# Optimization experiments

Hardware: AMD Instinct MI355X
Metric: run time of the kernel (lower is better)

Reference implementation:

```python
import jax, jax.numpy as jnp
import numpy as np

EPS = 1e-5

def _bn(x, g, b):
    # BatchNorm3d in training mode over (batch, spatial) dims; x: [B, C, N]
    mean = jnp.mean(x, axis=(0, 2), keepdims=True)
    var = jnp.var(x, axis=(0, 2), keepdims=True)
    return g[None, :, None] * (x - mean) * jax.lax.rsqrt(var + EPS) + b[None, :, None]


def setup_inputs() -> dict:
    key = jax.random.key(0)
    ks = jax.random.split(key, 6)
    B, C, N, K, H = 2, 128, 32768, 9, 512
    x = jax.random.normal(ks[0], (B, C, N, 1), dtype=jnp.float32)
    edge_index = jax.random.randint(ks[1], (2, B, N, K), 0, N, dtype=jnp.int32)
    s = 0.05
    return {
        "x": x,
        "edge_index": edge_index,
        "w_mr": jax.random.normal(ks[2], (C, 2 * C), dtype=jnp.float32) * s,
        "b_mr": jnp.zeros((C,), jnp.float32),
        "g_mr": jnp.ones((C,), jnp.float32),
        "be_mr": jnp.zeros((C,), jnp.float32),
        "w1": jax.random.normal(ks[3], (H, C), dtype=jnp.float32) * s,
        "b1": jnp.zeros((H,), jnp.float32),
        "g1": jnp.ones((H,), jnp.float32),
        "be1": jnp.zeros((H,), jnp.float32),
        "w2": jax.random.normal(ks[4], (C, H), dtype=jnp.float32) * s,
        "b2": jnp.zeros((C,), jnp.float32),
        "g2": jnp.ones((C,), jnp.float32),
        "be2": jnp.zeros((C,), jnp.float32),
    }


def reference(x, edge_index, w_mr, b_mr, g_mr, be_mr, w1, b1, g1, be1, w2, b2, g2, be2):
    # x: [B, C, N, 1], edge_index: [2, B, N, K]
    B, C, N, _ = x.shape
    x2 = x[..., 0]  # [B, C, N]

    # batched_index_select: gather node features along N for each (B, N, K) index
    gather = jax.vmap(lambda xb, ib: xb[:, ib])  # ([C,N],[N,K]) -> [C,N,K]
    x_i = gather(x2, edge_index[1])  # [B, C, N, K] center features
    x_j = gather(x2, edge_index[0])  # [B, C, N, K] neighbor features
    rel = jnp.max(x_j - x_i, axis=-1)  # max-relative reduction -> [B, C, N]

    # torch.cat([x.unsqueeze(2), rel.unsqueeze(2)], 2).reshape(B, 2C, N): interleaved channels
    feat = jnp.stack([x2, rel], axis=2).reshape(B, 2 * C, N)

    # BasicConv([2C, C]): Conv3d 1x1 -> BN -> ReLU
    y = jnp.einsum('oc,bcn->bon', w_mr, feat) + b_mr[None, :, None]
    y = jax.nn.relu(_bn(y, g_mr, be_mr))

    # FFN: conv1x1 C->H, BN, ReLU, conv1x1 H->C, BN, residual
    h = jnp.einsum('hc,bcn->bhn', w1, y) + b1[None, :, None]
    h = jax.nn.relu(_bn(h, g1, be1))
    out = jnp.einsum('ch,bhn->bcn', w2, h) + b2[None, :, None]
    out = _bn(out, g2, be2) + y
    return out  # [B, C, N]
```

## Files before the change

### kernel.cpp

```cpp
#include <hip/hip_runtime.h>
#include <hip/hip_bf16.h>
#include <cstddef>
#include <cstdint>

#define BB 2
#define CC 128
#define NN 32768
#define KNBR 9
#define HH 512
#define PP (BB * NN)
#define TWO_C 256
#define EPSBN 1e-5f

typedef __attribute__((ext_vector_type(4))) float f32x4;
typedef __attribute__((ext_vector_type(8))) short s16x8;

__device__ __forceinline__ float bf2f(unsigned int u) {
    return __uint_as_float(u << 16);
}
__device__ __forceinline__ unsigned short f2bf(float f) {
    unsigned int u = __float_as_uint(f);
    u += 0x7fffu + ((u >> 16) & 1u);
    return (unsigned short)(u >> 16);
}

__device__ __forceinline__ s16x8 bnrelu(s16x8 v, f32x4 sa0, f32x4 sa1,
                                        f32x4 sb0, f32x4 sb1) {
    union { s16x8 s; __hip_bfloat162 h[4]; } u;
    u.s = v;
#pragma unroll
    for (int q = 0; q < 4; q++) {
        const float2 f = __bfloat1622float2(u.h[q]);
        const float slo = (q < 2) ? sa0[2 * q] : sa1[2 * q - 4];
        const float shi = (q < 2) ? sa0[2 * q + 1] : sa1[2 * q - 3];
        const float tlo = (q < 2) ? sb0[2 * q] : sb1[2 * q - 4];
        const float thi = (q < 2) ? sb0[2 * q + 1] : sb1[2 * q - 3];
        u.h[q] = __float22bfloat162_rn(make_float2(
            fmaxf(fmaf(slo, f.x, tlo), 0.f), fmaxf(fmaf(shi, f.y, thi), 0.f)));
    }
    return u.s;
}


__global__ __launch_bounds__(256) void transpose_kernel(
    const float* __restrict__ x, unsigned short* __restrict__ xT) {
    __shared__ float t[32][129];
    const int b = blockIdx.y;
    const int n0 = blockIdx.x * 32;
    const int tid = threadIdx.x;
    {
        const int tn = tid % 32;
        const int cq = tid / 32;
        for (int c = cq; c < CC; c += 8)
            t[tn][c] = x[((size_t)b * CC + c) * NN + n0 + tn];
    }
    __syncthreads();
    {
        const int ct = tid % 128;
        const int nq = tid / 128;
        for (int nl = nq; nl < 32; nl += 2)
            xT[((size_t)b * NN + n0 + nl) * CC + ct] = f2bf(t[nl][ct]);
    }
}

__global__ __launch_bounds__(256) void gather_kernel(
    const unsigned short* __restrict__ xT, const int* __restrict__ ei,
    unsigned short* __restrict__ feat) {
    __shared__ unsigned short lds[16 * 264];
    const int p0 = blockIdx.x * 16;
    const int b = p0 >> 15;
    const int n0 = p0 & (NN - 1);
    const int tid = threadIdx.x;
    const int wv = tid >> 6, lane = tid & 63;
    const unsigned short* xb = xT + (size_t)b * NN * CC;

#pragma unroll
    for (int q = 0; q < 4; q++) {
        const int pl = wv * 4 + q;
        const int n = n0 + pl;
        const int* e0 = ei + ((size_t)b * NN + n) * KNBR;
        const int* e1 = ei + ((size_t)(BB + b) * NN + n) * KNBR;
        const unsigned int xv = *(const unsigned int*)(xb + (size_t)n * CC + lane * 2);
        float m0 = -INFINITY, m1 = -INFINITY;
#pragma unroll
        for (int k = 0; k < KNBR; k++) {
            const int j0 = e0[k], j1 = e1[k];
            const unsigned int va = *(const unsigned int*)(xb + (size_t)j0 * CC + lane * 2);
            const unsigned int vb = *(const unsigned int*)(xb + (size_t)j1 * CC + lane * 2);
            m0 = fmaxf(m0, bf2f(va & 0xffffu) - bf2f(vb & 0xffffu));
            m1 = fmaxf(m1, bf2f(va >> 16) - bf2f(vb >> 16));
        }
        ushort4 o;
        o.x = (unsigned short)(xv & 0xffffu);
        o.y = f2bf(m0);
        o.z = (unsigned short)(xv >> 16);
        o.w = f2bf(m1);
        *(ushort4*)(lds + pl * 264 + lane * 4) = o;
    }
    __syncthreads();
#pragma unroll
    for (int pass = 0; pass < 2; pass++) {
        const int s = pass * 256 + tid;
        const int kt = s >> 6, ln = s & 63;
        const int pl = ln & 15, kq = ln >> 4;
        const s16x8 v = *(const s16x8*)(lds + pl * 264 + kt * 32 + kq * 8);
        *(s16x8*)(feat + ((size_t)((p0 >> 4) * 8 + kt) * 64 + ln) * 8) = v;
    }
}

__global__ __launch_bounds__(256) void wconv_kernel(
    const float* __restrict__ w_mr, const float* __restrict__ w1,
    const float* __restrict__ w2, unsigned short* __restrict__ o_mr,
    unsigned short* __restrict__ o1, unsigned short* __restrict__ o2) {
    const int t = blockIdx.x * 256 + threadIdx.x;
    const float* src; unsigned short* dst; int K; int slot;
    if (t < 8192) { src = w1; dst = o1; K = 128; slot = t; }
    else if (t < 16384) { src = w2; dst = o2; K = 512; slot = t - 8192; }
    else if (t < 20480) { src = w_mr; dst = o_mr; K = 256; slot = t - 16384; }
    else return;
    const int lane = slot & 63;
    const int kt = (slot >> 6) % (K / 32);
    const int ot = (slot >> 6) / (K / 32);
    const int oc = ot * 16 + (lane & 15);
    const int k0 = kt * 32 + (lane >> 4) * 8;
    s16x8 v;
#pragma unroll
    for (int j = 0; j < 8; j++) v[j] = (short)f2bf(src[(size_t)oc * K + k0 + j]);
    *(s16x8*)(dst + (size_t)slot * 8) = v;
}

template <int KTOT, int OCB, int OC, bool ACT>
__global__ __launch_bounds__(256, 2) void sgemm2_kernel(
    const unsigned short* __restrict__ A,
    const unsigned short* __restrict__ W,
    const float* __restrict__ bias,
    const float* __restrict__ act,
    unsigned short* __restrict__ Cout,
    float* __restrict__ part) {
    constexpr int KT = KTOT / 32;
    constexpr int NTB = OCB / 16;
    constexpr int NTW = NTB / 2;
    constexpr int OCT32 = OC / 32;

    __shared__ __align__(16) unsigned short ALDS[4 * KT * 512];
    __shared__ float bs[4 * OCB];

    const int tid = threadIdx.x;
    const int w = tid >> 6, lane = tid & 63;
    const int mw = w >> 1, nw = w & 1;
    const int lm = lane & 15, lg = lane >> 4;
    const int pt0 = blockIdx.x * 4;
    const int ob = blockIdx.y * OCB;

    {
        const unsigned short* Asrc = A + (size_t)pt0 * KT * 512;
        s16x8 ar[KT];
#pragma unroll
        for (int i = 0; i < KT; i++)
            ar[i] = *(const s16x8*)(Asrc + (size_t)(i * 256 + tid) * 8);
#pragma unroll
        for (int i = 0; i < KT; i++)
            *(s16x8*)(ALDS + (size_t)(i * 256 + tid) * 8) = ar[i];
    }
    __syncthreads();

    f32x4 acc[2][NTW] = {};

#pragma unroll
    for (int kt = 0; kt < KT; kt++) {
        s16x8 bF[NTW];
#pragma unroll
        for (int n = 0; n < NTW; n++)
            bF[n] = *(const s16x8*)(
                W + ((size_t)(((ob >> 4) + nw * NTW + n) * KT + kt) * 64 + lane) * 8);
        s16x8 a0 = *(const s16x8*)(ALDS + (size_t)(((mw * 2 + 0) * KT + kt) * 64 + lane) * 8);
        s16x8 a1 = *(const s16x8*)(ALDS + (size_t)(((mw * 2 + 1) * KT + kt) * 64 + lane) * 8);
        if (ACT) {
            const int ke = kt * 32 + lg * 8;
            const f32x4 xa0 = *(const f32x4*)(act + ke);
            const f32x4 xa1 = *(const f32x4*)(act + ke + 4);
            const f32x4 xb0 = *(const f32x4*)(act + KTOT + ke);
            const f32x4 xb1 = *(const f32x4*)(act + KTOT + ke + 4);
            a0 = bnrelu(a0, xa0, xa1, xb0, xb1);
            a1 = bnrelu(a1, xa0, xa1, xb0, xb1);
        }
#pragma unroll
        for (int n = 0; n < NTW; n++) {
            acc[0][n] = __builtin_amdgcn_mfma_f32_16x16x32_bf16(a0, bF[n], acc[0][n], 0, 0, 0);
            acc[1][n] = __builtin_amdgcn_mfma_f32_16x16x32_bf16(a1, bF[n], acc[1][n], 0, 0, 0);
        }
    }
    __syncthreads();

    unsigned short* myct = ALDS + (size_t)w * (NTW / 2) * 512;
    float sA[NTW], sB[NTW], bo[NTW];
#pragma unroll
    for (int n = 0; n < NTW; n++) {
        sA[n] = 0.f; sB[n] = 0.f;
        bo[n] = bias[ob + nw * (OCB / 2) + n * 16 + lm];
    }
#pragma unroll
    for (int mi = 0; mi < 2; mi++) {
        const int ptile = pt0 + mw * 2 + mi;
#pragma unroll
        for (int n = 0; n < NTW; n++) {
            const int lbase = ((n & 1) * 2 + (lm >> 3)) * 16 + lg * 4;
            const int elem = lm & 7;
#pragma unroll
            for (int j = 0; j < 4; j++) {
                const float h = acc[mi][n][j] + bo[n];
                sA[n] += h;
                sB[n] = fmaf(h, h, sB[n]);
                myct[(size_t)((n >> 1) * 64 + lbase + j) * 8 + elem] = f2bf(h);
            }
        }
#pragma unroll
        for (int og = 0; og < NTW / 2; og++) {
            const s16x8 v = *(const s16x8*)(myct + (size_t)(og * 64 + lane) * 8);
            const int oct = ((ob + nw * (OCB / 2)) >> 5) + og;
            *(s16x8*)(Cout + ((size_t)(ptile * OCT32 + oct) * 64 + lane) * 8) = v;
        }
    }
#pragma unroll
    for (int n = 0; n < NTW; n++) {
        float a = sA[n], q = sB[n];
        a += __shfl_xor(a, 16); a += __shfl_xor(a, 32);
        q += __shfl_xor(q, 16); q += __shfl_xor(q, 32);
        if (lg == 0) {
            const int chl = nw * (OCB / 2) + n * 16 + lm;
            bs[(mw * 2 + 0) * OCB + chl] = a;
            bs[(mw * 2 + 1) * OCB + chl] = q;
        }
    }
    __syncthreads();
    if (tid < OCB) {
        const float s = bs[0 * OCB + tid] + bs[2 * OCB + tid];
        const float q = bs[1 * OCB + tid] + bs[3 * OCB + tid];
        const size_t o = ((size_t)blockIdx.y * gridDim.x + blockIdx.x) * 2 * OCB;
        part[o + tid] = s;
        part[o + OCB + tid] = q;
    }
}

template <int OCB, int GX>
__global__ __launch_bounds__(256) void reduce_kernel(
    const float* __restrict__ part, const float* __restrict__ g,
    const float* __restrict__ be, float* __restrict__ act, int OC, float invP) {
    __shared__ float ls[4], lq[4];
    const int c = blockIdx.x;
    const int by = c / OCB, co = c % OCB;
    const int tid = threadIdx.x;
    float s = 0.f, q = 0.f;
#pragma unroll
    for (int i = 0; i < GX / 256; i++) {
        const int bx = i * 256 + tid;
        const size_t o = (size_t)(by * GX + bx) * 2 * OCB;
        s += part[o + co];
        q += part[o + OCB + co];
    }
#pragma unroll
    for (int off = 32; off >= 1; off >>= 1) {
        s += __shfl_xor(s, off);
        q += __shfl_xor(q, off);
    }
    if ((tid & 63) == 0) { ls[tid >> 6] = s; lq[tid >> 6] = q; }
    __syncthreads();
    if (tid == 0) {
        s = ls[0] + ls[1] + ls[2] + ls[3];
        q = lq[0] + lq[1] + lq[2] + lq[3];
        const float mean = s * invP;
        const float var = q * invP - mean * mean;
        const float a = g[c] * rsqrtf(var + EPSBN);
        act[c] = a;
        act[OC + c] = be[c] - mean * a;
    }
}

__global__ __launch_bounds__(256) void final_kernel(
    const unsigned short* __restrict__ yF, const unsigned short* __restrict__ oF,
    const float* __restrict__ act1, const float* __restrict__ act3,
    float* __restrict__ out) {
    __shared__ float t[32][132];
    const int p0 = blockIdx.x * 32;
    const int b = p0 >> 15;
    const int n0 = p0 & (NN - 1);
    const int tid = threadIdx.x;
#pragma unroll
    for (int s = tid; s < 512; s += 256) {
        const int pt = s >> 8;
        const int kt = (s >> 6) & 3;
        const int lane = s & 63;
        const int nl = pt * 16 + (lane & 15);
        const int c0 = kt * 32 + (lane >> 4) * 8;
        const size_t off = ((size_t)(((p0 >> 4) + pt) * 4 + kt) * 64 + lane) * 8;
        const s16x8 yv = *(const s16x8*)(yF + off);
        const s16x8 ov = *(const s16x8*)(oF + off);
        const f32x4 a1lo = *(const f32x4*)(act1 + c0);
        const f32x4 a1hi = *(const f32x4*)(act1 + c0 + 4);
        const f32x4 b1lo = *(const f32x4*)(act1 + CC + c0);
        const f32x4 b1hi = *(const f32x4*)(act1 + CC + c0 + 4);
        const f32x4 a3lo = *(const f32x4*)(act3 + c0);
        const f32x4 a3hi = *(const f32x4*)(act3 + c0 + 4);
        const f32x4 b3lo = *(const f32x4*)(act3 + CC + c0);
        const f32x4 b3hi = *(const f32x4*)(act3 + CC + c0 + 4);
#pragma unroll
        for (int j = 0; j < 8; j++) {
            const float yf = bf2f((unsigned short)yv[j]);
            const float of = bf2f((unsigned short)ov[j]);
            const float a1 = (j < 4) ? a1lo[j] : a1hi[j - 4];
            const float b1 = (j < 4) ? b1lo[j] : b1hi[j - 4];
            const float a3 = (j < 4) ? a3lo[j] : a3hi[j - 4];
            const float b3 = (j < 4) ? b3lo[j] : b3hi[j - 4];
            t[nl][c0 + j] = fmaf(a3, of, b3) + fmaxf(fmaf(a1, yf, b1), 0.f);
        }
    }
    __syncthreads();
    const int tn = tid & 31;
    const int cq = tid >> 5;
    for (int c = cq; c < CC; c += 8)
        out[((size_t)b * CC + c) * NN + n0 + tn] = t[tn][c];
}

extern "C" void kernel_launch(void* const* d_in, const int* in_sizes, int n_in,
                              void* d_out, int out_size, void* d_ws, size_t ws_size,
                              hipStream_t stream) {
    const float* x     = (const float*)d_in[0];
    const int*   ei    = (const int*)d_in[1];
    const float* w_mr  = (const float*)d_in[2];
    const float* b_mr  = (const float*)d_in[3];
    const float* g_mr  = (const float*)d_in[4];
    const float* be_mr = (const float*)d_in[5];
    const float* w1    = (const float*)d_in[6];
    const float* b1    = (const float*)d_in[7];
    const float* g1    = (const float*)d_in[8];
    const float* be1   = (const float*)d_in[9];
    const float* w2    = (const float*)d_in[10];
    const float* b2    = (const float*)d_in[11];
    const float* g2    = (const float*)d_in[12];
    const float* be2   = (const float*)d_in[13];
    float* out = (float*)d_out;

    char* ws = (char*)d_ws;
    unsigned short* xT    = (unsigned short*)(ws + 0);
    unsigned short* featF = (unsigned short*)(ws + 16777216);
    unsigned short* yF    = (unsigned short*)(ws + 50331648);
    unsigned short* hF    = (unsigned short*)(ws + 67108864);
    unsigned short* oF    = (unsigned short*)(ws + 134217728);
    unsigned short* wmrF  = (unsigned short*)(ws + 150994944);
    unsigned short* w1F   = (unsigned short*)(ws + 151060480);
    unsigned short* w2F   = (unsigned short*)(ws + 151191552);
    float* act1  = (float*)(ws + 151322624);
    float* act2  = (float*)(ws + 151323648);
    float* act3  = (float*)(ws + 151327744);
    float* part1 = (float*)(ws + 67108864);
    float* part2 = (float*)(ws + 134217728);
    float* part3 = (float*)(ws + 16777216);

    const float invP = 1.0f / (float)PP;

    transpose_kernel<<<dim3(NN / 32, BB), 256, 0, stream>>>(x, xT);
    gather_kernel<<<PP / 16, 256, 0, stream>>>(xT, ei, featF);
    wconv_kernel<<<80, 256, 0, stream>>>(w_mr, w1, w2, wmrF, w1F, w2F);

    sgemm2_kernel<TWO_C, CC, CC, false><<<dim3(PP / 64, 1), 256, 0, stream>>>(
        featF, wmrF, b_mr, act1, yF, part1);
    reduce_kernel<CC, PP / 64><<<CC, 256, 0, stream>>>(
        part1, g_mr, be_mr, act1, CC, invP);

    sgemm2_kernel<CC, 256, HH, true><<<dim3(PP / 64, 2), 256, 0, stream>>>(
        yF, w1F, b1, act1, hF, part2);
    reduce_kernel<256, PP / 64><<<HH, 256, 0, stream>>>(
        part2, g1, be1, act2, HH, invP);

    sgemm2_kernel<HH, CC, CC, true><<<dim3(PP / 64, 1), 256, 0, stream>>>(
        hF, w2F, b2, act2, oF, part3);
    reduce_kernel<CC, PP / 64><<<CC, 256, 0, stream>>>(
        part3, g2, be2, act3, CC, invP);

    final_kernel<<<PP / 32, 256, 0, stream>>>(yF, oF, act1, act3, out);
}
```

Before: 155.2 us.

## Replace BN partial-sum reduce kernels with atomics and move BN-ReLU to A-tile load

Each GEMM block now accumulates its per-channel sum and sum-of-squares directly into a global stats buffer with atomicAdd, and a tiny finalize kernel computes the scale and shift. This replaces the per-block partial write and the separate reduce kernel. The weight conversion is folded into the transpose launch as extra blocks. BN+ReLU on the A operand is applied once when the tile is staged into LDS instead of on every MFMA k-step. Atomics make the float summation order nondeterministic and add contention, and a memset is needed each call.

New measurement: 218.8 us. 1.41x slower.

```diff
diff --git a/kernel.cpp b/kernel.cpp
--- a/kernel.cpp
+++ b/kernel.cpp
@@ -42,8 +42,30 @@
 }
 
 
-__global__ __launch_bounds__(256) void transpose_kernel(
-    const float* __restrict__ x, unsigned short* __restrict__ xT) {
+__global__ __launch_bounds__(256) void transpose_wconv_kernel(
+    const float* __restrict__ x, unsigned short* __restrict__ xT,
+    const float* __restrict__ w_mr, const float* __restrict__ w1,
+    const float* __restrict__ w2, unsigned short* __restrict__ o_mr,
+    unsigned short* __restrict__ o1, unsigned short* __restrict__ o2) {
+    if (blockIdx.x >= NN / 32) {
+        if (blockIdx.y != 0) return;
+        const int t = (blockIdx.x - NN / 32) * 256 + threadIdx.x;
+        const float* src; unsigned short* dst; int K; int slot;
+        if (t < 8192) { src = w1; dst = o1; K = 128; slot = t; }
+        else if (t < 16384) { src = w2; dst = o2; K = 512; slot = t - 8192; }
+        else if (t < 20480) { src = w_mr; dst = o_mr; K = 256; slot = t - 16384; }
+        else return;
+        const int lane = slot & 63;
+        const int kt = (slot >> 6) % (K / 32);
+        const int ot = (slot >> 6) / (K / 32);
+        const int oc = ot * 16 + (lane & 15);
+        const int k0 = kt * 32 + (lane >> 4) * 8;
+        s16x8 v;
+#pragma unroll
+        for (int j = 0; j < 8; j++) v[j] = (short)f2bf(src[(size_t)oc * K + k0 + j]);
+        *(s16x8*)(dst + (size_t)slot * 8) = v;
+        return;
+    }
     __shared__ float t[32][129];
     const int b = blockIdx.y;
     const int n0 = blockIdx.x * 32;
@@ -108,27 +130,6 @@
     }
 }
 
-__global__ __launch_bounds__(256) void wconv_kernel(
-    const float* __restrict__ w_mr, const float* __restrict__ w1,
-    const float* __restrict__ w2, unsigned short* __restrict__ o_mr,
-    unsigned short* __restrict__ o1, unsigned short* __restrict__ o2) {
-    const int t = blockIdx.x * 256 + threadIdx.x;
-    const float* src; unsigned short* dst; int K; int slot;
-    if (t < 8192) { src = w1; dst = o1; K = 128; slot = t; }
-    else if (t < 16384) { src = w2; dst = o2; K = 512; slot = t - 8192; }
-    else if (t < 20480) { src = w_mr; dst = o_mr; K = 256; slot = t - 16384; }
-    else return;
-    const int lane = slot & 63;
-    const int kt = (slot >> 6) % (K / 32);
-    const int ot = (slot >> 6) / (K / 32);
-    const int oc = ot * 16 + (lane & 15);
-    const int k0 = kt * 32 + (lane >> 4) * 8;
-    s16x8 v;
-#pragma unroll
-    for (int j = 0; j < 8; j++) v[j] = (short)f2bf(src[(size_t)oc * K + k0 + j]);
-    *(s16x8*)(dst + (size_t)slot * 8) = v;
-}
-
 template <int KTOT, int OCB, int OC, bool ACT>
 __global__ __launch_bounds__(256, 2) void sgemm2_kernel(
     const unsigned short* __restrict__ A,
@@ -136,7 +137,7 @@
     const float* __restrict__ bias,
     const float* __restrict__ act,
     unsigned short* __restrict__ Cout,
-    float* __restrict__ part) {
+    float* __restrict__ stats) {
     constexpr int KT = KTOT / 32;
     constexpr int NTB = OCB / 16;
     constexpr int NTW = NTB / 2;
@@ -158,6 +159,20 @@
 #pragma unroll
         for (int i = 0; i < KT; i++)
             ar[i] = *(const s16x8*)(Asrc + (size_t)(i * 256 + tid) * 8);
+        if (ACT) {
+#pragma unroll
+            for (int i = 0; i < KT; i++) {
+                const int s = i * 256 + tid;
+                const int kts = (s >> 6) % KT;
+                const int lgs = (s & 63) >> 4;
+                const int ke = kts * 32 + lgs * 8;
+                const f32x4 xa0 = *(const f32x4*)(act + ke);
+                const f32x4 xa1 = *(const f32x4*)(act + ke + 4);
+                const f32x4 xb0 = *(const f32x4*)(act + KTOT + ke);
+                const f32x4 xb1 = *(const f32x4*)(act + KTOT + ke + 4);
+                ar[i] = bnrelu(ar[i], xa0, xa1, xb0, xb1);
+            }
+        }
 #pragma unroll
         for (int i = 0; i < KT; i++)
             *(s16x8*)(ALDS + (size_t)(i * 256 + tid) * 8) = ar[i];
@@ -173,17 +188,8 @@
         for (int n = 0; n < NTW; n++)
             bF[n] = *(const s16x8*)(
                 W + ((size_t)(((ob >> 4) + nw * NTW + n) * KT + kt) * 64 + lane) * 8);
-        s16x8 a0 = *(const s16x8*)(ALDS + (size_t)(((mw * 2 + 0) * KT + kt) * 64 + lane) * 8);
-        s16x8 a1 = *(const s16x8*)(ALDS + (size_t)(((mw * 2 + 1) * KT + kt) * 64 + lane) * 8);
-        if (ACT) {
-            const int ke = kt * 32 + lg * 8;
-            const f32x4 xa0 = *(const f32x4*)(act + ke);
-            const f32x4 xa1 = *(const f32x4*)(act + ke + 4);
-            const f32x4 xb0 = *(const f32x4*)(act + KTOT + ke);
-            const f32x4 xb1 = *(const f32x4*)(act + KTOT + ke + 4);
-            a0 = bnrelu(a0, xa0, xa1, xb0, xb1);
-            a1 = bnrelu(a1, xa0, xa1, xb0, xb1);
-        }
+        const s16x8 a0 = *(const s16x8*)(ALDS + (size_t)(((mw * 2 + 0) * KT + kt) * 64 + lane) * 8);
+        const s16x8 a1 = *(const s16x8*)(ALDS + (size_t)(((mw * 2 + 1) * KT + kt) * 64 + lane) * 8);
 #pragma unroll
         for (int n = 0; n < NTW; n++) {
             acc[0][n] = __builtin_amdgcn_mfma_f32_16x16x32_bf16(a0, bF[n], acc[0][n], 0, 0, 0);
@@ -236,43 +242,22 @@
     if (tid < OCB) {
         const float s = bs[0 * OCB + tid] + bs[2 * OCB + tid];
         const float q = bs[1 * OCB + tid] + bs[3 * OCB + tid];
-        const size_t o = ((size_t)blockIdx.y * gridDim.x + blockIdx.x) * 2 * OCB;
-        part[o + tid] = s;
-        part[o + OCB + tid] = q;
-    }
-}
-
-template <int OCB, int GX>
-__global__ __launch_bounds__(256) void reduce_kernel(
-    const float* __restrict__ part, const float* __restrict__ g,
-    const float* __restrict__ be, float* __restrict__ act, int OC, float invP) {
-    __shared__ float ls[4], lq[4];
-    const int c = blockIdx.x;
-    const int by = c / OCB, co = c % OCB;
-    const int tid = threadIdx.x;
-    float s = 0.f, q = 0.f;
-#pragma unroll
-    for (int i = 0; i < GX / 256; i++) {
-        const int bx = i * 256 + tid;
-        const size_t o = (size_t)(by * GX + bx) * 2 * OCB;
-        s += part[o + co];
-        q += part[o + OCB + co];
-    }
-#pragma unroll
-    for (int off = 32; off >= 1; off >>= 1) {
-        s += __shfl_xor(s, off);
-        q += __shfl_xor(q, off);
-    }
-    if ((tid & 63) == 0) { ls[tid >> 6] = s; lq[tid >> 6] = q; }
-    __syncthreads();
-    if (tid == 0) {
-        s = ls[0] + ls[1] + ls[2] + ls[3];
-        q = lq[0] + lq[1] + lq[2] + lq[3];
-        const float mean = s * invP;
-        const float var = q * invP - mean * mean;
+        atomicAdd(&stats[ob + tid], s);
+        atomicAdd(&stats[OC + ob + tid], q);
+    }
+}
+
+__global__ void finalize_kernel(const float* __restrict__ stats,
+                                const float* __restrict__ g,
+                                const float* __restrict__ be,
+                                float* __restrict__ act, int CH, float invP) {
+    const int c = blockIdx.x * blockDim.x + threadIdx.x;
+    if (c < CH) {
+        const float mean = stats[c] * invP;
+        const float var = stats[CH + c] * invP - mean * mean;
         const float a = g[c] * rsqrtf(var + EPSBN);
         act[c] = a;
-        act[OC + c] = be[c] - mean * a;
+        act[CH + c] = be[c] - mean * a;
     }
 }
 
@@ -349,33 +334,32 @@
     unsigned short* wmrF  = (unsigned short*)(ws + 150994944);
     unsigned short* w1F   = (unsigned short*)(ws + 151060480);
     unsigned short* w2F   = (unsigned short*)(ws + 151191552);
-    float* act1  = (float*)(ws + 151322624);
-    float* act2  = (float*)(ws + 151323648);
-    float* act3  = (float*)(ws + 151327744);
-    float* part1 = (float*)(ws + 67108864);
-    float* part2 = (float*)(ws + 134217728);
-    float* part3 = (float*)(ws + 16777216);
+    float* stats1 = (float*)(ws + 151322624);
+    float* stats2 = (float*)(ws + 151323648);
+    float* stats3 = (float*)(ws + 151327744);
+    float* act1   = (float*)(ws + 151328768);
+    float* act2   = (float*)(ws + 151329792);
+    float* act3   = (float*)(ws + 151333888);
 
     const float invP = 1.0f / (float)PP;
 
-    transpose_kernel<<<dim3(NN / 32, BB), 256, 0, stream>>>(x, xT);
+    hipMemsetAsync(stats1, 0, 6144, stream);
+
+    transpose_wconv_kernel<<<dim3(NN / 32 + 80, BB), 256, 0, stream>>>(
+        x, xT, w_mr, w1, w2, wmrF, w1F, w2F);
     gather_kernel<<<PP / 16, 256, 0, stream>>>(xT, ei, featF);
-    wconv_kernel<<<80, 256, 0, stream>>>(w_mr, w1, w2, wmrF, w1F, w2F);
 
     sgemm2_kernel<TWO_C, CC, CC, false><<<dim3(PP / 64, 1), 256, 0, stream>>>(
-        featF, wmrF, b_mr, act1, yF, part1);
-    reduce_kernel<CC, PP / 64><<<CC, 256, 0, stream>>>(
-        part1, g_mr, be_mr, act1, CC, invP);
+        featF, wmrF, b_mr, act1, yF, stats1);
+    finalize_kernel<<<1, 256, 0, stream>>>(stats1, g_mr, be_mr, act1, CC, invP);
 
     sgemm2_kernel<CC, 256, HH, true><<<dim3(PP / 64, 2), 256, 0, stream>>>(
-        yF, w1F, b1, act1, hF, part2);
-    reduce_kernel<256, PP / 64><<<HH, 256, 0, stream>>>(
-        part2, g1, be1, act2, HH, invP);
+        yF, w1F, b1, act1, hF, stats2);
+    finalize_kernel<<<2, 256, 0, stream>>>(stats2, g1, be1, act2, HH, invP);
 
     sgemm2_kernel<HH, CC, CC, true><<<dim3(PP / 64, 1), 256, 0, stream>>>(
-        hF, w2F, b2, act2, oF, part3);
-    reduce_kernel<CC, PP / 64><<<CC, 256, 0, stream>>>(
-        part3, g2, be2, act3, CC, invP);
+        hF, w2F, b2, act2, oF, stats3);
+    finalize_kernel<<<1, 256, 0, stream>>>(stats3, g2, be2, act3, CC, invP);
 
     final_kernel<<<PP / 32, 256, 0, stream>>>(yF, oF, act1, act3, out);
 }
```
